# Kernel tuning notes

Hardware: AMD Instinct MI355X
Metric: run time of the kernel (lower is better)

Reference implementation:

```python
import jax, jax.numpy as jnp
import numpy as np

KSIZE = 7
LOSS_WEIGHT = 1.0


def _box_filter(x, ksize):
    # x: (N, 1, H, W) already reflect-padded -> valid conv with ones kernel
    kern = jnp.ones((1, 1, ksize, ksize), x.dtype)
    return jax.lax.conv_general_dilated(
        x, kern, window_strides=(1, 1), padding='VALID',
        dimension_numbers=('NCHW', 'OIHW', 'NCHW'))


def _local_var(residual, ksize):
    # unbiased variance over each ksize x ksize window (reflect padding),
    # computed via box-filtered sum and sum-of-squares (same math as
    # torch.var over unfolded windows, without materializing the windows).
    pad = (ksize - 1) // 2
    rp = jnp.pad(residual, ((0, 0), (0, 0), (pad, pad), (pad, pad)), mode='reflect')
    n = ksize * ksize
    s = _box_filter(rp, ksize)        # window sums
    ss = _box_filter(rp * rp, ksize)  # window sums of squares
    return (ss - s * s / n) / (n - 1)


def setup_inputs() -> dict:
    key = jax.random.key(0)
    k1, k2 = jax.random.split(key)
    shape = (16, 3, 512, 512)
    pred = jax.random.normal(k1, shape, dtype=jnp.float32)
    target = jax.random.normal(k2, shape, dtype=jnp.float32)
    return {"pred": pred, "target": target}


def reference(pred, target):
    # residual over channels: (N, 1, H, W)
    residual = jnp.sum(jnp.abs(target - pred), axis=1, keepdims=True)
    # patch-level weight: unbiased var over (C,H,W), ^(1/5)
    patch_w = jnp.var(residual, axis=(1, 2, 3), keepdims=True, ddof=1) ** 0.2
    # pixel-level weight: local unbiased variance in ksize window
    pixel_w = _local_var(residual, KSIZE)
    overall_weight = patch_w * pixel_w  # (N, 1, H, W), broadcasts over C
    # L1 criterion on weighted pred vs weighted target
    return jnp.mean(jnp.abs(overall_weight * pred - overall_weight * target)) * LOSS_WEIGHT
```

## Files before the change

kernel.cpp:

```cpp
#include <hip/hip_runtime.h>
#include <math.h>

#define N_IMG 16
#define C_CH 3
#define H_DIM 512
#define W_DIM 512
#define HW (H_DIM * W_DIM)
#define KS 7
#define PAD 3

#define TS 64
#define TILE (TS + 2 * PAD)
#define TSTRIDE 72
#define TPB 256
#define TILES_PER_IMG ((H_DIM / TS) * (W_DIM / TS))
#define NBLOCKS (N_IMG * TILES_PER_IMG)


__global__ __launch_bounds__(TPB) void k_fused(const float* __restrict__ pred,
                                               const float* __restrict__ targ,
                                               float* __restrict__ pr,
                                               float* __restrict__ pr2,
                                               float* __restrict__ pc) {
    __shared__ float tile[TILE * TSTRIDE];

    const int bid = blockIdx.x;
    const int n   = bid >> 6;
    const int t   = bid & 63;
    const int by  = t >> 3;
    const int bx  = t & 7;
    const int tid = threadIdx.x;

    const float* p0 = pred + (size_t)n * C_CH * HW;
    const float* p1 = p0 + HW;
    const float* p2 = p1 + HW;
    const float* q0 = targ + (size_t)n * C_CH * HW;
    const float* q1 = q0 + HW;
    const float* q2 = q1 + HW;

    const int y0 = by * TS - PAD;
    const int x0 = bx * TS - PAD;
#pragma unroll 4
    for (int it = 0; it < 19; ++it) {
        const int i  = tid + it * TPB;
        const int ly = i / TILE;
        const int lx = i - ly * TILE;
        int gy = y0 + ly;
        int gx = x0 + lx;
        gy = (gy < 0) ? -gy : ((gy >= H_DIM) ? (2 * H_DIM - 2 - gy) : gy);
        gx = (gx < 0) ? -gx : ((gx >= W_DIM) ? (2 * W_DIM - 2 - gx) : gx);
        const int off = gy * W_DIM + gx;
        tile[ly * TSTRIDE + lx] = fabsf(q0[off] - p0[off])
                                + fabsf(q1[off] - p1[off])
                                + fabsf(q2[off] - p2[off]);
    }
    if (tid < 36) {
        const int i  = tid + 19 * TPB;
        const int ly = i / TILE;
        const int lx = i - ly * TILE;
        int gy = y0 + ly;
        int gx = x0 + lx;
        gy = (gy < 0) ? -gy : ((gy >= H_DIM) ? (2 * H_DIM - 2 - gy) : gy);
        gx = (gx < 0) ? -gx : ((gx >= W_DIM) ? (2 * W_DIM - 2 - gx) : gx);
        const int off = gy * W_DIM + gx;
        tile[ly * TSTRIDE + lx] = fabsf(q0[off] - p0[off])
                                + fabsf(q1[off] - p1[off])
                                + fabsf(q2[off] - p2[off]);
    }
    __syncthreads();

    const int tx  = tid & 63;
    const int ty0 = (tid >> 6) << 4;

    float rS[KS], rSS[KS];
    float S = 0.f, SS = 0.f;
#pragma unroll
    for (int dy = 0; dy < KS; ++dy) {
        float s = 0.f, ss = 0.f;
#pragma unroll
        for (int j = 0; j < KS; ++j) {
            const float v = tile[(ty0 + dy) * TSTRIDE + tx + j];
            s  += v;
            ss += v * v;
        }
        rS[dy] = s; rSS[dy] = ss;
        S += s; SS += ss;
    }

    float acc_r = 0.f, acc_r2 = 0.f, acc_c = 0.f;

#pragma unroll
    for (int k = 0; k < 16; ++k) {
        if (k > 0) {
            float s = 0.f, ss = 0.f;
#pragma unroll
            for (int j = 0; j < KS; ++j) {
                const float v = tile[(ty0 + 6 + k) * TSTRIDE + tx + j];
                s  += v;
                ss += v * v;
            }
            const int slot = (k - 1) % KS;
            S  += s  - rS[slot];
            SS += ss - rSS[slot];
            rS[slot] = s; rSS[slot] = ss;
        }
        const float pix_var = (SS - S * S * (1.0f / 49.0f)) * (1.0f / 48.0f);
        const float center  = tile[(ty0 + 3 + k) * TSTRIDE + tx + 3];

        acc_r  += center;
        acc_r2 += center * center;
        acc_c  += pix_var * center;
    }

#pragma unroll
    for (int off = 32; off > 0; off >>= 1) {
        acc_r  += __shfl_down(acc_r,  off);
        acc_r2 += __shfl_down(acc_r2, off);
        acc_c  += __shfl_down(acc_c,  off);
    }
    __shared__ float sh_r[4], sh_r2[4], sh_c[4];
    const int lane = tid & 63;
    const int wave = tid >> 6;
    if (lane == 0) { sh_r[wave] = acc_r; sh_r2[wave] = acc_r2; sh_c[wave] = acc_c; }
    __syncthreads();
    if (tid == 0) {
        pr [bid] = sh_r [0] + sh_r [1] + sh_r [2] + sh_r [3];
        pr2[bid] = sh_r2[0] + sh_r2[1] + sh_r2[2] + sh_r2[3];
        pc [bid] = sh_c [0] + sh_c [1] + sh_c [2] + sh_c [3];
    }
}

__global__ void k_final(const float* __restrict__ pr,
                        const float* __restrict__ pr2,
                        const float* __restrict__ pc,
                        float* __restrict__ out) {
    __shared__ double sh[N_IMG];
    const int tid  = threadIdx.x;
    const int w    = tid >> 6;
    const int lane = tid & 63;

    double R = 0.0, R2 = 0.0, Cs = 0.0;
    if (lane < TILES_PER_IMG) {
        const int idx = w * TILES_PER_IMG + lane;
        R  = (double)pr[idx];
        R2 = (double)pr2[idx];
        Cs = (double)pc[idx];
    }
#pragma unroll
    for (int off = 32; off > 0; off >>= 1) {
        R  += __shfl_down(R,  off);
        R2 += __shfl_down(R2, off);
        Cs += __shfl_down(Cs, off);
    }
    if (lane == 0) {
        const double pvar = (R2 - R * R / (double)HW) / (double)(HW - 1);
        sh[w] = pow(pvar, 0.2) * Cs;
    }
    __syncthreads();
    if (tid == 0) {
        double s = 0.0;
        for (int i = 0; i < N_IMG; ++i) s += sh[i];
        out[0] = (float)(s / ((double)N_IMG * C_CH * HW));
    }
}

extern "C" void kernel_launch(void* const* d_in, const int* in_sizes, int n_in,
                              void* d_out, int out_size, void* d_ws, size_t ws_size,
                              hipStream_t stream) {
    const float* pred = (const float*)d_in[0];
    const float* targ = (const float*)d_in[1];

    float* pr  = (float*)d_ws;
    float* pr2 = pr  + NBLOCKS;
    float* pc  = pr2 + NBLOCKS;
    float* out = (float*)d_out;

    k_fused<<<NBLOCKS, TPB, 0, stream>>>(pred, targ, pr, pr2, pc);
    k_final<<<1, 1024, 0, stream>>>(pr, pr2, pc, out);
}
```

Before: 127.9 us.

## Vectorize interior tile loads and merge final reduction via cooperative grid sync

Interior tiles now load pred and target with float4 over a 72-column, 16-byte-aligned window with no reflect-index math. Boundary tiles keep the scalar reflect path, and the stencil indexing is shifted by one column to match the new alignment. The separate final-reduction kernel is replaced by a cooperative launch with a grid-wide sync, after which block 0 reduces the per-tile partials. This aims to cut load instruction count and one kernel launch, but it requires all 1024 blocks to be co-resident and adds grid-sync overhead.

```diff
diff --git a/kernel.cpp b/kernel.cpp
--- a/kernel.cpp
+++ b/kernel.cpp
@@ -1,5 +1,8 @@
 #include <hip/hip_runtime.h>
+#include <hip/hip_cooperative_groups.h>
 #include <math.h>
+
+namespace cg = cooperative_groups;
 
 #define N_IMG 16
 #define C_CH 3
@@ -10,19 +13,21 @@
 #define PAD 3
 
 #define TS 64
-#define TILE (TS + 2 * PAD)
+#define TROWS 70
+#define TCOLS 72
 #define TSTRIDE 72
 #define TPB 256
 #define TILES_PER_IMG ((H_DIM / TS) * (W_DIM / TS))
 #define NBLOCKS (N_IMG * TILES_PER_IMG)
 
 
-__global__ __launch_bounds__(TPB) void k_fused(const float* __restrict__ pred,
-                                               const float* __restrict__ targ,
-                                               float* __restrict__ pr,
-                                               float* __restrict__ pr2,
-                                               float* __restrict__ pc) {
-    __shared__ float tile[TILE * TSTRIDE];
+__global__ __launch_bounds__(TPB, 4) void k_all(const float* __restrict__ pred,
+                                                const float* __restrict__ targ,
+                                                float* __restrict__ pr,
+                                                float* __restrict__ pr2,
+                                                float* __restrict__ pc,
+                                                float* __restrict__ out) {
+    __shared__ float tile[TROWS * TSTRIDE];
 
     const int bid = blockIdx.x;
     const int n   = bid >> 6;
@@ -39,33 +44,47 @@
     const float* q2 = q1 + HW;
 
     const int y0 = by * TS - PAD;
-    const int x0 = bx * TS - PAD;
+    const int xa = bx * TS - 4;
+
+    if (by >= 1 && by <= 6 && bx >= 1 && bx <= 6) {
+#pragma unroll
+        for (int it = 0; it < 5; ++it) {
+            const int i = tid + it * TPB;
+            if (i < TROWS * 18) {
+                const int r = i / 18;
+                const int g = i - r * 18;
+                const int goff = (y0 + r) * W_DIM + xa + g * 4;
+                const float4 a0 = *(const float4*)(p0 + goff);
+                const float4 a1 = *(const float4*)(p1 + goff);
+                const float4 a2 = *(const float4*)(p2 + goff);
+                const float4 b0 = *(const float4*)(q0 + goff);
+                const float4 b1 = *(const float4*)(q1 + goff);
+                const float4 b2 = *(const float4*)(q2 + goff);
+                float4 res;
+                res.x = fabsf(b0.x - a0.x) + fabsf(b1.x - a1.x) + fabsf(b2.x - a2.x);
+                res.y = fabsf(b0.y - a0.y) + fabsf(b1.y - a1.y) + fabsf(b2.y - a2.y);
+                res.z = fabsf(b0.z - a0.z) + fabsf(b1.z - a1.z) + fabsf(b2.z - a2.z);
+                res.w = fabsf(b0.w - a0.w) + fabsf(b1.w - a1.w) + fabsf(b2.w - a2.w);
+                *(float4*)&tile[r * TSTRIDE + g * 4] = res;
+            }
+        }
+    } else {
 #pragma unroll 4
-    for (int it = 0; it < 19; ++it) {
-        const int i  = tid + it * TPB;
-        const int ly = i / TILE;
-        const int lx = i - ly * TILE;
-        int gy = y0 + ly;
-        int gx = x0 + lx;
-        gy = (gy < 0) ? -gy : ((gy >= H_DIM) ? (2 * H_DIM - 2 - gy) : gy);
-        gx = (gx < 0) ? -gx : ((gx >= W_DIM) ? (2 * W_DIM - 2 - gx) : gx);
-        const int off = gy * W_DIM + gx;
-        tile[ly * TSTRIDE + lx] = fabsf(q0[off] - p0[off])
-                                + fabsf(q1[off] - p1[off])
-                                + fabsf(q2[off] - p2[off]);
-    }
-    if (tid < 36) {
-        const int i  = tid + 19 * TPB;
-        const int ly = i / TILE;
-        const int lx = i - ly * TILE;
-        int gy = y0 + ly;
-        int gx = x0 + lx;
-        gy = (gy < 0) ? -gy : ((gy >= H_DIM) ? (2 * H_DIM - 2 - gy) : gy);
-        gx = (gx < 0) ? -gx : ((gx >= W_DIM) ? (2 * W_DIM - 2 - gx) : gx);
-        const int off = gy * W_DIM + gx;
-        tile[ly * TSTRIDE + lx] = fabsf(q0[off] - p0[off])
-                                + fabsf(q1[off] - p1[off])
-                                + fabsf(q2[off] - p2[off]);
+        for (int it = 0; it < 20; ++it) {
+            const int i = tid + it * TPB;
+            if (i < TROWS * TCOLS) {
+                const int ly = i / TCOLS;
+                const int lx = i - ly * TCOLS;
+                int gy = y0 + ly;
+                int gx = xa + lx;
+                gy = (gy < 0) ? -gy : ((gy >= H_DIM) ? (2 * H_DIM - 2 - gy) : gy);
+                gx = (gx < 0) ? -gx : ((gx >= W_DIM) ? (2 * W_DIM - 2 - gx) : gx);
+                const int off = gy * W_DIM + gx;
+                tile[ly * TSTRIDE + lx] = fabsf(q0[off] - p0[off])
+                                        + fabsf(q1[off] - p1[off])
+                                        + fabsf(q2[off] - p2[off]);
+            }
+        }
     }
     __syncthreads();
 
@@ -79,7 +98,7 @@
         float s = 0.f, ss = 0.f;
 #pragma unroll
         for (int j = 0; j < KS; ++j) {
-            const float v = tile[(ty0 + dy) * TSTRIDE + tx + j];
+            const float v = tile[(ty0 + dy) * TSTRIDE + tx + 1 + j];
             s  += v;
             ss += v * v;
         }
@@ -95,7 +114,7 @@
             float s = 0.f, ss = 0.f;
 #pragma unroll
             for (int j = 0; j < KS; ++j) {
-                const float v = tile[(ty0 + 6 + k) * TSTRIDE + tx + j];
+                const float v = tile[(ty0 + 6 + k) * TSTRIDE + tx + 1 + j];
                 s  += v;
                 ss += v * v;
             }
@@ -105,7 +124,7 @@
             rS[slot] = s; rSS[slot] = ss;
         }
         const float pix_var = (SS - S * S * (1.0f / 49.0f)) * (1.0f / 48.0f);
-        const float center  = tile[(ty0 + 3 + k) * TSTRIDE + tx + 3];
+        const float center  = tile[(ty0 + 3 + k) * TSTRIDE + tx + 4];
 
         acc_r  += center;
         acc_r2 += center * center;
@@ -128,39 +147,28 @@
         pr2[bid] = sh_r2[0] + sh_r2[1] + sh_r2[2] + sh_r2[3];
         pc [bid] = sh_c [0] + sh_c [1] + sh_c [2] + sh_c [3];
     }
-}
 
-__global__ void k_final(const float* __restrict__ pr,
-                        const float* __restrict__ pr2,
-                        const float* __restrict__ pc,
-                        float* __restrict__ out) {
-    __shared__ double sh[N_IMG];
-    const int tid  = threadIdx.x;
-    const int w    = tid >> 6;
-    const int lane = tid & 63;
+    cg::this_grid().sync();
 
-    double R = 0.0, R2 = 0.0, Cs = 0.0;
-    if (lane < TILES_PER_IMG) {
-        const int idx = w * TILES_PER_IMG + lane;
-        R  = (double)pr[idx];
-        R2 = (double)pr2[idx];
-        Cs = (double)pc[idx];
-    }
+    if (bid == 0) {
+        double v = 0.0;
+        if (tid < N_IMG) {
+            double R = 0.0, R2 = 0.0, Cs = 0.0;
+#pragma unroll 8
+            for (int i = 0; i < TILES_PER_IMG; ++i) {
+                const int idx = tid * TILES_PER_IMG + i;
+                R  += (double)pr[idx];
+                R2 += (double)pr2[idx];
+                Cs += (double)pc[idx];
+            }
+            const double pvar = (R2 - R * R / (double)HW) / (double)(HW - 1);
+            v = pow(pvar, 0.2) * Cs;
+        }
+        if (tid < 64) {
 #pragma unroll
-    for (int off = 32; off > 0; off >>= 1) {
-        R  += __shfl_down(R,  off);
-        R2 += __shfl_down(R2, off);
-        Cs += __shfl_down(Cs, off);
-    }
-    if (lane == 0) {
-        const double pvar = (R2 - R * R / (double)HW) / (double)(HW - 1);
-        sh[w] = pow(pvar, 0.2) * Cs;
-    }
-    __syncthreads();
-    if (tid == 0) {
-        double s = 0.0;
-        for (int i = 0; i < N_IMG; ++i) s += sh[i];
-        out[0] = (float)(s / ((double)N_IMG * C_CH * HW));
+            for (int off = 8; off > 0; off >>= 1) v += __shfl_down(v, off);
+            if (tid == 0) out[0] = (float)(v / ((double)N_IMG * C_CH * HW));
+        }
     }
 }
 
@@ -175,6 +183,8 @@
     float* pc  = pr2 + NBLOCKS;
     float* out = (float*)d_out;
 
-    k_fused<<<NBLOCKS, TPB, 0, stream>>>(pred, targ, pr, pr2, pc);
-    k_final<<<1, 1024, 0, stream>>>(pr, pr2, pc, out);
+    void* args[] = {(void*)&pred, (void*)&targ, (void*)&pr,
+                    (void*)&pr2, (void*)&pc, (void*)&out};
+    hipLaunchCooperativeKernel((const void*)k_all, dim3(NBLOCKS), dim3(TPB),
+                               args, 0, stream);
 }
```

Result: slower. 248.7 us (+94.4%).

## Halve tile height, vectorize residual loads with float4, raise occupancy hint

Applied to the files above, without the earlier changes.

Tiles shrink from 64x64 to 64x32 pixels, which doubles the block count to 2048, and each thread's sliding window now covers 8 rows instead of 16. The halo load is realigned to 4-element groups, so interior pixels are read with float4 loads of pred and target, with a scalar reflect path only at the image edges. The launch bounds now ask for 8 blocks per CU, and the final reduction is adapted to 128 tiles per image. The aim is more parallelism and wider memory transactions, at the cost of a larger share of halo rows that are recomputed per tile.

```diff
diff --git a/kernel.cpp b/kernel.cpp
--- a/kernel.cpp
+++ b/kernel.cpp
@@ -9,24 +9,34 @@
 #define KS 7
 #define PAD 3
 
-#define TS 64
-#define TILE (TS + 2 * PAD)
+#define TSX 64
+#define TSY 32
+#define TROWS (TSY + 2 * PAD)
+#define TCOLS 72
 #define TSTRIDE 72
 #define TPB 256
-#define TILES_PER_IMG ((H_DIM / TS) * (W_DIM / TS))
+#define NGROUPS (TROWS * 18)
+#define TILES_PER_IMG ((H_DIM / TSY) * (W_DIM / TSX))
 #define NBLOCKS (N_IMG * TILES_PER_IMG)
 
 
-__global__ __launch_bounds__(TPB) void k_fused(const float* __restrict__ pred,
-                                               const float* __restrict__ targ,
-                                               float* __restrict__ pr,
-                                               float* __restrict__ pr2,
-                                               float* __restrict__ pc) {
-    __shared__ float tile[TILE * TSTRIDE];
+__device__ __forceinline__ int reflect_y(int gy) {
+    return (gy < 0) ? -gy : ((gy >= H_DIM) ? (2 * H_DIM - 2 - gy) : gy);
+}
+__device__ __forceinline__ int reflect_x(int gx) {
+    return (gx < 0) ? -gx : ((gx >= W_DIM) ? (2 * W_DIM - 2 - gx) : gx);
+}
+
+__global__ __launch_bounds__(TPB, 8) void k_fused(const float* __restrict__ pred,
+                                                  const float* __restrict__ targ,
+                                                  float* __restrict__ pr,
+                                                  float* __restrict__ pr2,
+                                                  float* __restrict__ pc) {
+    __shared__ float tile[TROWS * TSTRIDE];
 
     const int bid = blockIdx.x;
-    const int n   = bid >> 6;
-    const int t   = bid & 63;
+    const int n   = bid >> 7;
+    const int t   = bid & 127;
     const int by  = t >> 3;
     const int bx  = t & 7;
     const int tid = threadIdx.x;
@@ -38,39 +48,47 @@
     const float* q1 = q0 + HW;
     const float* q2 = q1 + HW;
 
-    const int y0 = by * TS - PAD;
-    const int x0 = bx * TS - PAD;
-#pragma unroll 4
-    for (int it = 0; it < 19; ++it) {
-        const int i  = tid + it * TPB;
-        const int ly = i / TILE;
-        const int lx = i - ly * TILE;
-        int gy = y0 + ly;
-        int gx = x0 + lx;
-        gy = (gy < 0) ? -gy : ((gy >= H_DIM) ? (2 * H_DIM - 2 - gy) : gy);
-        gx = (gx < 0) ? -gx : ((gx >= W_DIM) ? (2 * W_DIM - 2 - gx) : gx);
-        const int off = gy * W_DIM + gx;
-        tile[ly * TSTRIDE + lx] = fabsf(q0[off] - p0[off])
-                                + fabsf(q1[off] - p1[off])
-                                + fabsf(q2[off] - p2[off]);
-    }
-    if (tid < 36) {
-        const int i  = tid + 19 * TPB;
-        const int ly = i / TILE;
-        const int lx = i - ly * TILE;
-        int gy = y0 + ly;
-        int gx = x0 + lx;
-        gy = (gy < 0) ? -gy : ((gy >= H_DIM) ? (2 * H_DIM - 2 - gy) : gy);
-        gx = (gx < 0) ? -gx : ((gx >= W_DIM) ? (2 * W_DIM - 2 - gx) : gx);
-        const int off = gy * W_DIM + gx;
-        tile[ly * TSTRIDE + lx] = fabsf(q0[off] - p0[off])
-                                + fabsf(q1[off] - p1[off])
-                                + fabsf(q2[off] - p2[off]);
+    const int y0 = by * TSY - PAD;
+    const int xa = bx * TSX - 4;
+
+#pragma unroll
+    for (int it = 0; it < 3; ++it) {
+        const int i = tid + it * TPB;
+        if (i < NGROUPS) {
+            const int r  = i / 18;
+            const int g  = i - r * 18;
+            const int gy = reflect_y(y0 + r);
+            const int gx0 = xa + 4 * g;
+            if (gx0 >= 0 && gx0 <= (W_DIM - 4)) {
+                const int goff = gy * W_DIM + gx0;
+                const float4 a0 = *(const float4*)(p0 + goff);
+                const float4 a1 = *(const float4*)(p1 + goff);
+                const float4 a2 = *(const float4*)(p2 + goff);
+                const float4 b0 = *(const float4*)(q0 + goff);
+                const float4 b1 = *(const float4*)(q1 + goff);
+                const float4 b2 = *(const float4*)(q2 + goff);
+                float4 res;
+                res.x = fabsf(b0.x - a0.x) + fabsf(b1.x - a1.x) + fabsf(b2.x - a2.x);
+                res.y = fabsf(b0.y - a0.y) + fabsf(b1.y - a1.y) + fabsf(b2.y - a2.y);
+                res.z = fabsf(b0.z - a0.z) + fabsf(b1.z - a1.z) + fabsf(b2.z - a2.z);
+                res.w = fabsf(b0.w - a0.w) + fabsf(b1.w - a1.w) + fabsf(b2.w - a2.w);
+                *(float4*)&tile[r * TSTRIDE + g * 4] = res;
+            } else {
+#pragma unroll
+                for (int j = 0; j < 4; ++j) {
+                    const int gx = reflect_x(gx0 + j);
+                    const int off = gy * W_DIM + gx;
+                    tile[r * TSTRIDE + g * 4 + j] = fabsf(q0[off] - p0[off])
+                                                  + fabsf(q1[off] - p1[off])
+                                                  + fabsf(q2[off] - p2[off]);
+                }
+            }
+        }
     }
     __syncthreads();
 
     const int tx  = tid & 63;
-    const int ty0 = (tid >> 6) << 4;
+    const int ty0 = (tid >> 6) << 3;
 
     float rS[KS], rSS[KS];
     float S = 0.f, SS = 0.f;
@@ -79,7 +97,7 @@
         float s = 0.f, ss = 0.f;
 #pragma unroll
         for (int j = 0; j < KS; ++j) {
-            const float v = tile[(ty0 + dy) * TSTRIDE + tx + j];
+            const float v = tile[(ty0 + dy) * TSTRIDE + tx + 1 + j];
             s  += v;
             ss += v * v;
         }
@@ -90,22 +108,22 @@
     float acc_r = 0.f, acc_r2 = 0.f, acc_c = 0.f;
 
 #pragma unroll
-    for (int k = 0; k < 16; ++k) {
+    for (int k = 0; k < 8; ++k) {
         if (k > 0) {
             float s = 0.f, ss = 0.f;
 #pragma unroll
             for (int j = 0; j < KS; ++j) {
-                const float v = tile[(ty0 + 6 + k) * TSTRIDE + tx + j];
+                const float v = tile[(ty0 + 6 + k) * TSTRIDE + tx + 1 + j];
                 s  += v;
                 ss += v * v;
             }
-            const int slot = (k - 1) % KS;
+            const int slot = k - 1;
             S  += s  - rS[slot];
             SS += ss - rSS[slot];
             rS[slot] = s; rSS[slot] = ss;
         }
         const float pix_var = (SS - S * S * (1.0f / 49.0f)) * (1.0f / 48.0f);
-        const float center  = tile[(ty0 + 3 + k) * TSTRIDE + tx + 3];
+        const float center  = tile[(ty0 + 3 + k) * TSTRIDE + tx + 4];
 
         acc_r  += center;
         acc_r2 += center * center;
@@ -139,13 +157,10 @@
     const int w    = tid >> 6;
     const int lane = tid & 63;
 
-    double R = 0.0, R2 = 0.0, Cs = 0.0;
-    if (lane < TILES_PER_IMG) {
-        const int idx = w * TILES_PER_IMG + lane;
-        R  = (double)pr[idx];
-        R2 = (double)pr2[idx];
-        Cs = (double)pc[idx];
-    }
+    const int i0 = w * TILES_PER_IMG + lane;
+    double R  = (double)pr [i0] + (double)pr [i0 + 64];
+    double R2 = (double)pr2[i0] + (double)pr2[i0 + 64];
+    double Cs = (double)pc [i0] + (double)pc [i0 + 64];
 #pragma unroll
     for (int off = 32; off > 0; off >>= 1) {
         R  += __shfl_down(R,  off);
```

New measurement: 131.3 us. 1.03x slower.

## Stream rows per wave with register-pipelined loads and running column sums

Applied to the files above, without the earlier changes.

Replaces the block-wide shared-memory halo tile with per-wave vertical strips of 64 columns by 32 rows. Each lane keeps an 8-entry register ring of residuals and running vertical 7-row sums. The next row's six inputs are prefetched into double-buffered registers while the current row is processed, and horizontal 7-tap sums go through a small per-wave LDS buffer with no block barriers. This targets the redundant halo recompute, the separate load phase before compute, and the __syncthreads cost. In exchange it adds partial-lane dual loads for the halo columns, an extra vertical halo per strip, and more partial sums for the final reduction.

```diff
diff --git a/kernel.cpp b/kernel.cpp
--- a/kernel.cpp
+++ b/kernel.cpp
@@ -7,109 +7,135 @@
 #define W_DIM 512
 #define HW (H_DIM * W_DIM)
 #define KS 7
-#define PAD 3
 
-#define TS 64
-#define TILE (TS + 2 * PAD)
-#define TSTRIDE 72
+#define SPANW 64
+#define RSTRIP 32
+#define WAVES_PER_IMG 128
+#define NSTRIPS (N_IMG * WAVES_PER_IMG)
 #define TPB 256
-#define TILES_PER_IMG ((H_DIM / TS) * (W_DIM / TS))
-#define NBLOCKS (N_IMG * TILES_PER_IMG)
+#define NBLK (NSTRIPS / 4)
 
+__device__ __forceinline__ int reflect_y(int y) {
+    return (y < 0) ? -y : ((y >= H_DIM) ? (2 * H_DIM - 2 - y) : y);
+}
+__device__ __forceinline__ int reflect_x(int x) {
+    return (x < 0) ? -x : ((x >= W_DIM) ? (2 * W_DIM - 2 - x) : x);
+}
+
+#define STEP(RR, RI, CUR, NXT, CURD, NXTD)                                    \
+  {                                                                           \
+    const int gy_ = reflect_y((RR) + 4);                                      \
+    const int on_ = gy_ * W_DIM + colp;                                       \
+    NXT[0] = p0[on_]; NXT[1] = p1[on_]; NXT[2] = p2[on_];                     \
+    NXT[3] = q0[on_]; NXT[4] = q1[on_]; NXT[5] = q2[on_];                     \
+    if (dual) {                                                               \
+      const int od_ = gy_ * W_DIM + cold;                                     \
+      NXTD[0] = p0[od_]; NXTD[1] = p1[od_]; NXTD[2] = p2[od_];                \
+      NXTD[3] = q0[od_]; NXTD[4] = q1[od_]; NXTD[5] = q2[od_];                \
+    }                                                                         \
+    const float vn_ = fabsf(CUR[3] - CUR[0]) + fabsf(CUR[4] - CUR[1])         \
+                    + fabsf(CUR[5] - CUR[2]);                                 \
+    const float vo_ = v1r[((RI) + 4) & 7];                      \
+    S1 += vn_ - vo_; SS1 += vn_ * vn_ - vo_ * vo_;                            \
+    v1r[((RI) + 3) & 7] = vn_;                     \
+    if (dual) {                                                               \
+      const float wn_ = fabsf(CURD[3] - CURD[0]) + fabsf(CURD[4] - CURD[1])   \
+                      + fabsf(CURD[5] - CURD[2]);                             \
+      const float wo_ = v2r[((RI) + 4) & 7];                                  \
+      S2 += wn_ - wo_; SS2 += wn_ * wn_ - wo_ * wo_;                          \
+      v2r[((RI) + 3) & 7] = wn_;                                              \
+    }                                                                         \
+    cs[wave][lane] = make_float2(S1, SS1);                                    \
+    if (dual) cs[wave][64 + lane] = make_float2(S2, SS2);                     \
+    asm volatile("s_waitcnt lgkmcnt(0)" ::: "memory");                        \
+    __builtin_amdgcn_sched_barrier(0);                                        \
+    float wS_ = 0.f, wSS_ = 0.f;                                              \
+    _Pragma("unroll")                                                         \
+    for (int j_ = 0; j_ < 7; ++j_) {                                          \
+      const float2 t_ = cs[wave][lane + j_];                                  \
+      wS_ += t_.x; wSS_ += t_.y;                                              \
+    }                                                                         \
+    const float c1_ = __shfl(v1r[(RI) & 7], (lane + 3) & 63);                 \
+    const float c2_ = __shfl(v2r[(RI) & 7], (lane - 61) & 63);                \
+    const float ctr_ = (lane < 61) ? c1_ : c2_;                               \
+    const float pv_ = (wSS_ - wS_ * wS_ * (1.0f / 49.0f)) * (1.0f / 48.0f);   \
+    acc_r += ctr_; acc_r2 += ctr_ * ctr_; acc_c += pv_ * ctr_;                \
+  }
 
 __global__ __launch_bounds__(TPB) void k_fused(const float* __restrict__ pred,
                                                const float* __restrict__ targ,
                                                float* __restrict__ pr,
                                                float* __restrict__ pr2,
                                                float* __restrict__ pc) {
-    __shared__ float tile[TILE * TSTRIDE];
+    __shared__ float2 cs[4][72];
 
-    const int bid = blockIdx.x;
-    const int n   = bid >> 6;
-    const int t   = bid & 63;
-    const int by  = t >> 3;
-    const int bx  = t & 7;
-    const int tid = threadIdx.x;
+    const int wg   = ((blockIdx.x & 7) << 6) | (blockIdx.x >> 3);
+    const int tid  = threadIdx.x;
+    const int wave = tid >> 6;
+    const int lane = tid & 63;
+    const int sid  = wg * 4 + wave;
+    const int img  = sid >> 7;
+    const int rem  = sid & 127;
+    const int x0   = (rem & 7) * SPANW;
+    const int r0   = (rem >> 3) * RSTRIP;
 
-    const float* p0 = pred + (size_t)n * C_CH * HW;
+    const float* p0 = pred + (size_t)img * C_CH * HW;
     const float* p1 = p0 + HW;
     const float* p2 = p1 + HW;
-    const float* q0 = targ + (size_t)n * C_CH * HW;
+    const float* q0 = targ + (size_t)img * C_CH * HW;
     const float* q1 = q0 + HW;
     const float* q2 = q1 + HW;
 
-    const int y0 = by * TS - PAD;
-    const int x0 = bx * TS - PAD;
-#pragma unroll 4
-    for (int it = 0; it < 19; ++it) {
-        const int i  = tid + it * TPB;
-        const int ly = i / TILE;
-        const int lx = i - ly * TILE;
-        int gy = y0 + ly;
-        int gx = x0 + lx;
-        gy = (gy < 0) ? -gy : ((gy >= H_DIM) ? (2 * H_DIM - 2 - gy) : gy);
-        gx = (gx < 0) ? -gx : ((gx >= W_DIM) ? (2 * W_DIM - 2 - gx) : gx);
-        const int off = gy * W_DIM + gx;
-        tile[ly * TSTRIDE + lx] = fabsf(q0[off] - p0[off])
-                                + fabsf(q1[off] - p1[off])
-                                + fabsf(q2[off] - p2[off]);
+    const int  colp = reflect_x(x0 - 3 + lane);
+    const int  cold = reflect_x(x0 + 61 + lane);
+    const bool dual = (lane < 6);
+
+    float v1r[8] = {0, 0, 0, 0, 0, 0, 0, 0};
+    float v2r[8] = {0, 0, 0, 0, 0, 0, 0, 0};
+    float S1 = 0.f, SS1 = 0.f, S2 = 0.f, SS2 = 0.f;
+
+#pragma unroll
+    for (int i = 0; i < 8; ++i) {
+        const int gy = reflect_y(r0 - 5 + i);
+        const int o  = gy * W_DIM + colp;
+        const float v = fabsf(q0[o] - p0[o]) + fabsf(q1[o] - p1[o])
+                      + fabsf(q2[o] - p2[o]);
+        v1r[(i + 3) & 7] = v;
+        if (i != 0) { S1 += v; SS1 += v * v; }
+        if (dual) {
+            const int o2 = gy * W_DIM + cold;
+            const float w = fabsf(q0[o2] - p0[o2]) + fabsf(q1[o2] - p1[o2])
+                          + fabsf(q2[o2] - p2[o2]);
+            v2r[(i + 3) & 7] = w;
+            if (i != 0) { S2 += w; SS2 += w * w; }
+        }
     }
-    if (tid < 36) {
-        const int i  = tid + 19 * TPB;
-        const int ly = i / TILE;
-        const int lx = i - ly * TILE;
-        int gy = y0 + ly;
-        int gx = x0 + lx;
-        gy = (gy < 0) ? -gy : ((gy >= H_DIM) ? (2 * H_DIM - 2 - gy) : gy);
-        gx = (gx < 0) ? -gx : ((gx >= W_DIM) ? (2 * W_DIM - 2 - gx) : gx);
-        const int off = gy * W_DIM + gx;
-        tile[ly * TSTRIDE + lx] = fabsf(q0[off] - p0[off])
-                                + fabsf(q1[off] - p1[off])
-                                + fabsf(q2[off] - p2[off]);
-    }
-    __syncthreads();
 
-    const int tx  = tid & 63;
-    const int ty0 = (tid >> 6) << 4;
-
-    float rS[KS], rSS[KS];
-    float S = 0.f, SS = 0.f;
-#pragma unroll
-    for (int dy = 0; dy < KS; ++dy) {
-        float s = 0.f, ss = 0.f;
-#pragma unroll
-        for (int j = 0; j < KS; ++j) {
-            const float v = tile[(ty0 + dy) * TSTRIDE + tx + j];
-            s  += v;
-            ss += v * v;
+    float ra[6], rb[6], da[6], db[6];
+    {
+        const int gy = reflect_y(r0 + 3);
+        const int o  = gy * W_DIM + colp;
+        ra[0] = p0[o]; ra[1] = p1[o]; ra[2] = p2[o];
+        ra[3] = q0[o]; ra[4] = q1[o]; ra[5] = q2[o];
+        if (dual) {
+            const int o2 = gy * W_DIM + cold;
+            da[0] = p0[o2]; da[1] = p1[o2]; da[2] = p2[o2];
+            da[3] = q0[o2]; da[4] = q1[o2]; da[5] = q2[o2];
         }
-        rS[dy] = s; rSS[dy] = ss;
-        S += s; SS += ss;
     }
 
     float acc_r = 0.f, acc_r2 = 0.f, acc_c = 0.f;
 
-#pragma unroll
-    for (int k = 0; k < 16; ++k) {
-        if (k > 0) {
-            float s = 0.f, ss = 0.f;
-#pragma unroll
-            for (int j = 0; j < KS; ++j) {
-                const float v = tile[(ty0 + 6 + k) * TSTRIDE + tx + j];
-                s  += v;
-                ss += v * v;
-            }
-            const int slot = (k - 1) % KS;
-            S  += s  - rS[slot];
-            SS += ss - rSS[slot];
-            rS[slot] = s; rSS[slot] = ss;
-        }
-        const float pix_var = (SS - S * S * (1.0f / 49.0f)) * (1.0f / 48.0f);
-        const float center  = tile[(ty0 + 3 + k) * TSTRIDE + tx + 3];
-
-        acc_r  += center;
-        acc_r2 += center * center;
-        acc_c  += pix_var * center;
+    for (int ro = 0; ro < RSTRIP / 8; ++ro) {
+        const int rb8 = r0 + ro * 8;
+        STEP(rb8 + 0, 0, ra, rb, da, db)
+        STEP(rb8 + 1, 1, rb, ra, db, da)
+        STEP(rb8 + 2, 2, ra, rb, da, db)
+        STEP(rb8 + 3, 3, rb, ra, db, da)
+        STEP(rb8 + 4, 4, ra, rb, da, db)
+        STEP(rb8 + 5, 5, rb, ra, db, da)
+        STEP(rb8 + 6, 6, ra, rb, da, db)
+        STEP(rb8 + 7, 7, rb, ra, db, da)
     }
 
 #pragma unroll
@@ -118,16 +144,7 @@
         acc_r2 += __shfl_down(acc_r2, off);
         acc_c  += __shfl_down(acc_c,  off);
     }
-    __shared__ float sh_r[4], sh_r2[4], sh_c[4];
-    const int lane = tid & 63;
-    const int wave = tid >> 6;
-    if (lane == 0) { sh_r[wave] = acc_r; sh_r2[wave] = acc_r2; sh_c[wave] = acc_c; }
-    __syncthreads();
-    if (tid == 0) {
-        pr [bid] = sh_r [0] + sh_r [1] + sh_r [2] + sh_r [3];
-        pr2[bid] = sh_r2[0] + sh_r2[1] + sh_r2[2] + sh_r2[3];
-        pc [bid] = sh_c [0] + sh_c [1] + sh_c [2] + sh_c [3];
-    }
+    if (lane == 0) { pr[sid] = acc_r; pr2[sid] = acc_r2; pc[sid] = acc_c; }
 }
 
 __global__ void k_final(const float* __restrict__ pr,
@@ -139,13 +156,10 @@
     const int w    = tid >> 6;
     const int lane = tid & 63;
 
-    double R = 0.0, R2 = 0.0, Cs = 0.0;
-    if (lane < TILES_PER_IMG) {
-        const int idx = w * TILES_PER_IMG + lane;
-        R  = (double)pr[idx];
-        R2 = (double)pr2[idx];
-        Cs = (double)pc[idx];
-    }
+    const int i0 = w * WAVES_PER_IMG + lane;
+    double R  = (double)pr [i0] + (double)pr [i0 + 64];
+    double R2 = (double)pr2[i0] + (double)pr2[i0 + 64];
+    double Cs = (double)pc [i0] + (double)pc [i0 + 64];
 #pragma unroll
     for (int off = 32; off > 0; off >>= 1) {
         R  += __shfl_down(R,  off);
@@ -171,10 +185,10 @@
     const float* targ = (const float*)d_in[1];
 
     float* pr  = (float*)d_ws;
-    float* pr2 = pr  + NBLOCKS;
-    float* pc  = pr2 + NBLOCKS;
+    float* pr2 = pr  + NSTRIPS;
+    float* pc  = pr2 + NSTRIPS;
     float* out = (float*)d_out;
 
-    k_fused<<<NBLOCKS, TPB, 0, stream>>>(pred, targ, pr, pr2, pc);
+    k_fused<<<NBLK, TPB, 0, stream>>>(pred, targ, pr, pr2, pc);
     k_final<<<1, 1024, 0, stream>>>(pr, pr2, pc, out);
 }
```

Result: slower. 133.7 us (+4.5%).
